# Performance work log

Hardware: AMD Instinct MI355X
Metric: run time of the kernel (lower is better)

## Reference

```python
import jax, jax.numpy as jnp
import numpy as np

N = 50000
E = 800000
IN_DIM = 256
OUT_DIM = 128
HEADS = 4
D_K = OUT_DIM // HEADS  # 32
BETA = 1.0  # beta_init, requires_grad=False (constant)
NEG_SLOPE = 0.2
EPS = 1e-12


def setup_inputs() -> dict:
    key = jax.random.key(0)
    k = jax.random.split(key, 8)
    H = jax.random.normal(k[0], (N, IN_DIM), dtype=jnp.float32)
    edge_index = jax.random.randint(k[1], (2, E), 0, N, dtype=jnp.int64)
    sim1_edge = jax.random.normal(k[2], (E,), dtype=jnp.float32)
    # Parameters (torch nn.Linear stores weight as (out, in); y = x @ W.T)
    W = jax.random.normal(k[3], (HEADS * D_K, IN_DIM), dtype=jnp.float32) * (1.0 / np.sqrt(IN_DIM))
    a_src = jax.random.normal(k[4], (HEADS, D_K), dtype=jnp.float32)
    a_dst = jax.random.normal(k[5], (HEADS, D_K), dtype=jnp.float32)
    msg_lin_w = jax.random.normal(k[6], (D_K, D_K), dtype=jnp.float32) * (1.0 / np.sqrt(D_K))
    return {"H": H, "edge_index": edge_index, "sim1_edge": sim1_edge,
            "W": W, "a_src": a_src, "a_dst": a_dst, "msg_lin_w": msg_lin_w}


def reference(H, edge_index, sim1_edge, W, a_src, a_dst, msg_lin_w):
    n = H.shape[0]
    H_proj = (H @ W.T).reshape(n, HEADS, D_K)           # [N, h, d_k]
    src, dst = edge_index[0], edge_index[1]
    h_src = H_proj[src]                                  # [E, h, d_k]
    h_dst = H_proj[dst]                                  # [E, h, d_k]
    # per-edge attention logits (struct + semantic)
    e = (jnp.einsum('ehd,hd->eh', h_src, a_src)
         + jnp.einsum('ehd,hd->eh', h_dst, a_dst)
         + BETA * sim1_edge[:, None])                    # [E, h]
    e = jnp.where(e >= 0, e, NEG_SLOPE * e)              # LeakyReLU(0.2)
    # global (per-head) max for stabilization, matching original e.max(dim=0)
    e = e - jnp.max(e, axis=0, keepdims=True)
    exp_e = jnp.exp(e)                                   # [E, h]
    denom = jax.ops.segment_sum(exp_e, dst, num_segments=n)  # [N, h]
    alpha = exp_e / (denom[dst] + EPS)                   # [E, h]  (dropout p=0 -> identity)
    m = alpha[:, :, None] * h_src                        # [E, h, d_k]
    out = jax.ops.segment_sum(m, dst, num_segments=n)    # [N, h, d_k]
    out_h = out.reshape(n, HEADS * D_K)                  # concat=True
    msg_base = jnp.einsum('ehd,od->eho', h_src, msg_lin_w).mean(axis=1)  # [E, d_k]
    alpha_mean = alpha.mean(axis=1)                      # [E]
    return out_h, alpha_mean, msg_base
```

## Files before the change

kernel.cpp:

```cpp
#include <hip/hip_runtime.h>
#include <hip/hip_bf16.h>
#include <hip/hip_fp16.h>
#include <float.h>

#define HEADS 4
#define DK 32

static constexpr float kBeta = 1.0f;
static constexpr float kNeg  = 0.2f;
static constexpr float kEps  = 1e-12f;

typedef __bf16 bf16x8 __attribute__((ext_vector_type(8)));
typedef float  f32x4  __attribute__((ext_vector_type(4)));

__device__ __forceinline__ float bf2f(unsigned short v) {
  return __uint_as_float((unsigned)v << 16);
}
__device__ __forceinline__ unsigned short f2bf(float f) {
  unsigned u = __float_as_uint(f);
  unsigned r = u + 0x7FFFu + ((u >> 16) & 1u);
  return (unsigned short)(r >> 16);
}
__device__ __forceinline__ float2 bfp2(unsigned u) {
  return make_float2(__uint_as_float(u << 16), __uint_as_float(u & 0xFFFF0000u));
}
__device__ __forceinline__ unsigned fkey(float x) {
  unsigned u = __float_as_uint(x);
  return (u & 0x80000000u) ? ~u : (u | 0x80000000u);
}
__device__ __forceinline__ float funkey(unsigned k) {
  unsigned u = (k & 0x80000000u) ? (k & 0x7fffffffu) : ~k;
  return __uint_as_float(u);
}
__device__ __forceinline__ bf16x8 as8(uint4 v) {
  union { uint4 u; bf16x8 b; } x; x.u = v; return x.b;
}

__global__ __launch_bounds__(256) void k_detect(const int* __restrict__ ei32,
                                                const unsigned* __restrict__ Hw,
                                                int* __restrict__ eflag,
                                                int* __restrict__ dflag,
                                                int E, int nw) {
  int i = blockIdx.x * 256 + threadIdx.x;
  if (i < 4096 && 2 * i + 1 < 2 * E && ei32[2 * i + 1] != 0) atomicOr(eflag, 1);
  if (i < nw && ((Hw[i] >> 7) & 0xFFu) == 0xFFu) atomicOr(dflag, 1);
}

__global__ __launch_bounds__(256) void k_cvt(const int* __restrict__ ei32,
                                             const int* __restrict__ eflag,
                                             int* __restrict__ src_i,
                                             int* __restrict__ dst_i,
                                             int* __restrict__ deg, int E) {
  int i = blockIdx.x * 256 + threadIdx.x;
  if (i >= E) return;
  int s, d;
  if (*eflag) { s = ei32[i];     d = ei32[E + i]; }
  else        { s = ei32[2 * i]; d = ei32[2 * E + 2 * i]; }
  src_i[i] = s;
  dst_i[i] = d;
  atomicAdd(deg + d, 1);
}

__global__ __launch_bounds__(256) void k_params(const void* __restrict__ a_src,
                                                const void* __restrict__ a_dst,
                                                const void* __restrict__ msg_w,
                                                float* __restrict__ af,
                                                float* __restrict__ msgwf,
                                                const int* __restrict__ dflag) {
  int i = blockIdx.x * 256 + threadIdx.x;
  int dt = *dflag;
  if (i < 128) {
    af[i] = dt ? ((const float*)a_src)[i] : bf2f(((const unsigned short*)a_src)[i]);
  } else if (i < 256) {
    int j = i - 128;
    af[i] = dt ? ((const float*)a_dst)[j] : bf2f(((const unsigned short*)a_dst)[j]);
  } else if (i < 1280) {
    int j = i - 256;
    msgwf[j] = dt ? ((const float*)msg_w)[j] : bf2f(((const unsigned short*)msg_w)[j]);
  }
}

__global__ __launch_bounds__(256) void k_wpack(const void* __restrict__ in,
                                               unsigned short* __restrict__ Bhi,
                                               unsigned short* __restrict__ Blo,
                                               const int* __restrict__ dflag, int n) {
  int i = blockIdx.x * 256 + threadIdx.x;
  if (i >= n) return;
  int r = i >> 8, c = i & 255;
  float v = (*dflag) ? ((const float*)in)[i] : bf2f(((const unsigned short*)in)[i]);
  unsigned short hb = f2bf(v);
  unsigned short lb = f2bf(v - bf2f(hb));
  int kt = c >> 5, ct = r >> 4;
  int lane = (((c >> 3) & 3) << 4) | (r & 15);
  int idx = ((kt * 8 + ct) * 64 + lane) * 8 + (c & 7);
  Bhi[idx] = hb;
  Blo[idx] = lb;
}

__global__ __launch_bounds__(256) void k_scan1(const int* __restrict__ deg,
                                               int* __restrict__ bsum, int N) {
  const int t = threadIdx.x;
  int i = blockIdx.x * 256 + t;
  int v = (i < N) ? deg[i] : 0;
#pragma unroll
  for (int off = 32; off; off >>= 1) v += __shfl_xor(v, off);
  __shared__ int red[4];
  if ((t & 63) == 0) red[t >> 6] = v;
  __syncthreads();
  if (t == 0) bsum[blockIdx.x] = red[0] + red[1] + red[2] + red[3];
}
__global__ __launch_bounds__(1024) void k_scan2(int* __restrict__ bsum, int nb) {
  __shared__ int part[1024];
  const int t = threadIdx.x;
  part[t] = (t < nb) ? bsum[t] : 0;
  __syncthreads();
  int own = part[t];
  for (int off = 1; off < 1024; off <<= 1) {
    int v = (t >= off) ? part[t - off] : 0;
    __syncthreads();
    part[t] += v;
    __syncthreads();
  }
  if (t < nb) bsum[t] = part[t] - own;
}
__global__ __launch_bounds__(256) void k_scan3(const int* __restrict__ deg,
                                               const int* __restrict__ bsum,
                                               int* __restrict__ row_ptr,
                                               int* __restrict__ cursor, int N) {
  __shared__ int part[256];
  const int t = threadIdx.x;
  int i = blockIdx.x * 256 + t;
  int v = (i < N) ? deg[i] : 0;
  part[t] = v;
  __syncthreads();
  for (int off = 1; off < 256; off <<= 1) {
    int x = (t >= off) ? part[t - off] : 0;
    __syncthreads();
    part[t] += x;
    __syncthreads();
  }
  int excl = part[t] - v + bsum[blockIdx.x];
  if (i < N) {
    row_ptr[i] = excl;
    cursor[i]  = excl;
    if (i == N - 1) row_ptr[N] = excl + v;
  }
}

__global__ __launch_bounds__(256) void k_fill(const int* __restrict__ dst,
                                              int* __restrict__ cursor,
                                              int* __restrict__ eidx, int E) {
  int e = blockIdx.x * 256 + threadIdx.x;
  if (e >= E) return;
  int pos = atomicAdd(cursor + dst[e], 1);
  eidx[pos] = e;
}

__global__ __launch_bounds__(256) void k_proj(const void* __restrict__ Hraw,
                                              const unsigned short* __restrict__ Bhi,
                                              const unsigned short* __restrict__ Blo,
                                              const int* __restrict__ dflag,
                                              float* __restrict__ Hproj, int N) {
  __shared__ uint4 lds4[4096];
  const int t = threadIdx.x;
  const int nb = blockIdx.x * 64;
  const int dt = *dflag;
  if (dt) {
    const float4* __restrict__ H4 = (const float4*)Hraw;
#pragma unroll
    for (int it = 0; it < 8; ++it) {
      int c = it * 256 + t;
      int row = c >> 5, k8 = c & 31;
      int gr = nb + row;
      float4 v0 = make_float4(0.f, 0.f, 0.f, 0.f), v1 = v0;
      if (gr < N) {
        v0 = H4[(size_t)gr * 64 + k8 * 2];
        v1 = H4[(size_t)gr * 64 + k8 * 2 + 1];
      }
      float f[8] = {v0.x, v0.y, v0.z, v0.w, v1.x, v1.y, v1.z, v1.w};
      unsigned hi[8], lo[8];
#pragma unroll
      for (int j = 0; j < 8; ++j) {
        unsigned short hb = f2bf(f[j]);
        hi[j] = hb;
        lo[j] = f2bf(f[j] - bf2f(hb));
      }
      int slot = (k8 * 64 + row) ^ (k8 & 7);
      lds4[slot] = make_uint4(hi[0] | (hi[1] << 16), hi[2] | (hi[3] << 16),
                              hi[4] | (hi[5] << 16), hi[6] | (hi[7] << 16));
      lds4[2048 + slot] = make_uint4(lo[0] | (lo[1] << 16), lo[2] | (lo[3] << 16),
                                     lo[4] | (lo[5] << 16), lo[6] | (lo[7] << 16));
    }
  } else {
    const uint4* __restrict__ H8 = (const uint4*)Hraw;
#pragma unroll
    for (int it = 0; it < 8; ++it) {
      int c = it * 256 + t;
      int row = c >> 5, k8 = c & 31;
      int gr = nb + row;
      uint4 v = make_uint4(0u, 0u, 0u, 0u);
      if (gr < N) v = H8[(size_t)gr * 32 + k8];
      lds4[(k8 * 64 + row) ^ (k8 & 7)] = v;
    }
  }
  __syncthreads();

  const int l = t & 63;
  const int wrow = (t >> 6) * 16;
  f32x4 acc[8];
#pragma unroll
  for (int ct = 0; ct < 8; ++ct) acc[ct] = (f32x4){0.f, 0.f, 0.f, 0.f};
  const uint4* __restrict__ Bh4 = (const uint4*)Bhi;
  const uint4* __restrict__ Bl4 = (const uint4*)Blo;
  if (dt) {
#pragma unroll 2
    for (int kt = 0; kt < 8; ++kt) {
      int k8 = kt * 4 + (l >> 4);
      int slot = (k8 * 64 + wrow + (l & 15)) ^ (k8 & 7);
      bf16x8 ah = as8(lds4[slot]);
      bf16x8 al = as8(lds4[2048 + slot]);
#pragma unroll
      for (int ct = 0; ct < 8; ++ct) {
        bf16x8 bh = as8(Bh4[(kt * 8 + ct) * 64 + l]);
        bf16x8 bl = as8(Bl4[(kt * 8 + ct) * 64 + l]);
        acc[ct] = __builtin_amdgcn_mfma_f32_16x16x32_bf16(ah, bh, acc[ct], 0, 0, 0);
        acc[ct] = __builtin_amdgcn_mfma_f32_16x16x32_bf16(ah, bl, acc[ct], 0, 0, 0);
        acc[ct] = __builtin_amdgcn_mfma_f32_16x16x32_bf16(al, bh, acc[ct], 0, 0, 0);
      }
    }
  } else {
#pragma unroll 2
    for (int kt = 0; kt < 8; ++kt) {
      int k8 = kt * 4 + (l >> 4);
      int slot = (k8 * 64 + wrow + (l & 15)) ^ (k8 & 7);
      bf16x8 ah = as8(lds4[slot]);
#pragma unroll
      for (int ct = 0; ct < 8; ++ct) {
        bf16x8 bh = as8(Bh4[(kt * 8 + ct) * 64 + l]);
        acc[ct] = __builtin_amdgcn_mfma_f32_16x16x32_bf16(ah, bh, acc[ct], 0, 0, 0);
      }
    }
  }
#pragma unroll
  for (int ct = 0; ct < 8; ++ct) {
#pragma unroll
    for (int r = 0; r < 4; ++r) {
      int grow = nb + wrow + (l >> 4) * 4 + r;
      if (grow < N) Hproj[(size_t)grow * 128 + ct * 16 + (l & 15)] = acc[ct][r];
    }
  }
}

__global__ __launch_bounds__(256) void k_node(const float* __restrict__ Hproj,
                                              const float* __restrict__ af,
                                              const float* __restrict__ msgwf,
                                              float* __restrict__ s_src,
                                              float* __restrict__ s_dst,
                                              __half* __restrict__ msgb,
                                              __half* __restrict__ Hb, int N) {
  const int l = threadIdx.x & 63;
  const int wb = threadIdx.x >> 6;
  const int n = (blockIdx.x << 2) + wb;
  if (n >= N) return;
  const float* row = Hproj + (size_t)n * 128;
  float h0 = row[l], h1 = row[64 + l];
  Hb[(size_t)n * 128 + l]      = __float2half(h0);
  Hb[(size_t)n * 128 + 64 + l] = __float2half(h1);
  float p0 = h0 * af[l],       p1 = h1 * af[64 + l];
  float q0 = h0 * af[128 + l], q1 = h1 * af[192 + l];
#pragma unroll
  for (int off = 16; off; off >>= 1) {
    p0 += __shfl_xor(p0, off);
    p1 += __shfl_xor(p1, off);
    q0 += __shfl_xor(q0, off);
    q1 += __shfl_xor(q1, off);
  }
  if (l == 0)  { s_src[n*4+0] = p0; s_src[n*4+2] = p1; s_dst[n*4+0] = q0; s_dst[n*4+2] = q1; }
  if (l == 32) { s_src[n*4+1] = p0; s_src[n*4+3] = p1; s_dst[n*4+1] = q0; s_dst[n*4+3] = q1; }
  float t4 = h0 + __shfl_xor(h0, 32) + h1 + __shfl_xor(h1, 32);
  float hbar = 0.25f * t4;
  if (l < DK) {
    float acc = 0.f;
#pragma unroll
    for (int d = 0; d < DK; ++d) acc += __shfl(hbar, d) * msgwf[l * DK + d];
    msgb[(size_t)n * DK + l] = __float2half(acc);
  }
}

__global__ __launch_bounds__(256) void k_logits(const int* __restrict__ src,
                                                const int* __restrict__ dst,
                                                const void* __restrict__ sim1,
                                                const int* __restrict__ dflag,
                                                const float* __restrict__ s_src,
                                                const float* __restrict__ s_dst,
                                                unsigned* __restrict__ gmax, int E) {
  const int e = blockIdx.x * 256 + threadIdx.x;
  float m0 = -FLT_MAX, m1 = -FLT_MAX, m2 = -FLT_MAX, m3 = -FLT_MAX;
  if (e < E) {
    int s = src[e], d = dst[e];
    float4 ss = *(const float4*)(s_src + (size_t)s * 4);
    float4 sd = *(const float4*)(s_dst + (size_t)d * 4);
    float sv = (*dflag) ? ((const float*)sim1)[e] : bf2f(((const unsigned short*)sim1)[e]);
    float b = kBeta * sv;
    float e0 = ss.x + sd.x + b; e0 = (e0 >= 0.f) ? e0 : kNeg * e0;
    float e1 = ss.y + sd.y + b; e1 = (e1 >= 0.f) ? e1 : kNeg * e1;
    float e2 = ss.z + sd.z + b; e2 = (e2 >= 0.f) ? e2 : kNeg * e2;
    float e3 = ss.w + sd.w + b; e3 = (e3 >= 0.f) ? e3 : kNeg * e3;
    m0 = e0; m1 = e1; m2 = e2; m3 = e3;
  }
#pragma unroll
  for (int off = 32; off; off >>= 1) {
    m0 = fmaxf(m0, __shfl_xor(m0, off));
    m1 = fmaxf(m1, __shfl_xor(m1, off));
    m2 = fmaxf(m2, __shfl_xor(m2, off));
    m3 = fmaxf(m3, __shfl_xor(m3, off));
  }
  __shared__ float red[4][4];
  if ((threadIdx.x & 63) == 0) {
    int w = threadIdx.x >> 6;
    red[w][0] = m0; red[w][1] = m1; red[w][2] = m2; red[w][3] = m3;
  }
  __syncthreads();
  if (threadIdx.x < 4) {
    int h = threadIdx.x;
    float mm = fmaxf(fmaxf(red[0][h], red[1][h]), fmaxf(red[2][h], red[3][h]));
    atomicMax(gmax + h, fkey(mm));
  }
}

__global__ __launch_bounds__(256) void k_msg(const int* __restrict__ src,
                                             const __half2* __restrict__ msgb2,
                                             const int* __restrict__ dflag,
                                             void* __restrict__ d_out,
                                             int N, int E) {
  long long tid = (long long)blockIdx.x * 256 + threadIdx.x;
  if (tid >= (long long)E * 16) return;
  int e = (int)(tid >> 4), jp = (int)(tid & 15);
  __half2 hv = msgb2[(size_t)src[e] * 16 + jp];
  float2 f = __half22float2(hv);
  const size_t msg_off = (size_t)N * 128 + (size_t)E;
  if (*dflag) {
    *(float2*)&((float*)d_out)[msg_off + (size_t)e * 32 + 2 * jp] = f;
  } else {
    __hip_bfloat162 b = __float22bfloat162_rn(f);
    *(__hip_bfloat162*)((__hip_bfloat16*)d_out + msg_off + (size_t)e * 32 + 2 * jp) = b;
  }
}

__global__ __launch_bounds__(256) void k_out(const int* __restrict__ row_ptr,
                                             const int* __restrict__ eidx,
                                             const int* __restrict__ src,
                                             const void* __restrict__ sim1,
                                             const float* __restrict__ s_src,
                                             const float* __restrict__ s_dst,
                                             const unsigned* __restrict__ gmax,
                                             const unsigned* __restrict__ Hb_u,
                                             const int* __restrict__ dflag,
                                             void* __restrict__ d_out, int N, int E) {
  const int n = (int)((blockIdx.x * 256 + threadIdx.x) >> 6);
  const int l = threadIdx.x & 63;
  if (n >= N) return;
  const int beg = row_ptr[n];
  const int deg = row_ptr[n + 1] - beg;
  const int dt = *dflag;
  const float m0 = funkey(gmax[0]), m1 = funkey(gmax[1]);
  const float m2 = funkey(gmax[2]), m3 = funkey(gmax[3]);
  const float4 sd = *(const float4*)(s_dst + (size_t)n * 4);
  const size_t alpha_off = (size_t)N * 128;
  float accx = 0.f, accy = 0.f;
  float4 dn = make_float4(0.f, 0.f, 0.f, 0.f);
  int eid = 0, s = 0;
  float4 ev = make_float4(0.f, 0.f, 0.f, 0.f);
  const bool small = (deg <= 64);
  if (small) {
    if (l < deg) {
      eid = eidx[beg + l];
      s = src[eid];
      float4 ss = *(const float4*)(s_src + (size_t)s * 4);
      float sv = dt ? ((const float*)sim1)[eid] : bf2f(((const unsigned short*)sim1)[eid]);
      float e0 = ss.x + sd.x + sv; e0 = (e0 >= 0.f) ? e0 : kNeg * e0;
      float e1 = ss.y + sd.y + sv; e1 = (e1 >= 0.f) ? e1 : kNeg * e1;
      float e2 = ss.z + sd.z + sv; e2 = (e2 >= 0.f) ? e2 : kNeg * e2;
      float e3 = ss.w + sd.w + sv; e3 = (e3 >= 0.f) ? e3 : kNeg * e3;
      ev = make_float4(expf(e0 - m0), expf(e1 - m1), expf(e2 - m2), expf(e3 - m3));
      dn = ev;
    }
  } else {
    for (int base = 0; base < deg; base += 64) {
      if (base + l < deg) {
        int e2i = eidx[beg + base + l];
        int s2 = src[e2i];
        float4 ss = *(const float4*)(s_src + (size_t)s2 * 4);
        float sv = dt ? ((const float*)sim1)[e2i] : bf2f(((const unsigned short*)sim1)[e2i]);
        float e0 = ss.x + sd.x + sv; e0 = (e0 >= 0.f) ? e0 : kNeg * e0;
        float e1 = ss.y + sd.y + sv; e1 = (e1 >= 0.f) ? e1 : kNeg * e1;
        float e2 = ss.z + sd.z + sv; e2 = (e2 >= 0.f) ? e2 : kNeg * e2;
        float e3 = ss.w + sd.w + sv; e3 = (e3 >= 0.f) ? e3 : kNeg * e3;
        dn.x += expf(e0 - m0); dn.y += expf(e1 - m1);
        dn.z += expf(e2 - m2); dn.w += expf(e3 - m3);
      }
    }
  }
#pragma unroll
  for (int off = 32; off; off >>= 1) {
    dn.x += __shfl_xor(dn.x, off);
    dn.y += __shfl_xor(dn.y, off);
    dn.z += __shfl_xor(dn.z, off);
    dn.w += __shfl_xor(dn.w, off);
  }
  const float i0 = 1.f / (dn.x + kEps), i1 = 1.f / (dn.y + kEps);
  const float i2 = 1.f / (dn.z + kEps), i3 = 1.f / (dn.w + kEps);
  const float myinv = (l < 32) ? ((l < 16) ? i0 : i1) : ((l < 48) ? i2 : i3);
  if (small) {
    if (l < deg) {
      float am = 0.25f * (ev.x * i0 + ev.y * i1 + ev.z * i2 + ev.w * i3);
      if (dt) ((float*)d_out)[alpha_off + eid] = am;
      else    ((__hip_bfloat16*)d_out)[alpha_off + eid] = __float2bfloat16(am);
    }
    for (int i = 0; i < deg; ++i) {
      int si = __shfl(s, i);
      float ax = __shfl(ev.x, i), ay = __shfl(ev.y, i);
      float az = __shfl(ev.z, i), aw = __shfl(ev.w, i);
      float aa = ((l < 32) ? ((l < 16) ? ax : ay) : ((l < 48) ? az : aw)) * myinv;
      unsigned u = Hb_u[(size_t)si * 64 + l];
      float2 f = __half22float2(*(const __half2*)&u);
      accx += aa * f.x;
      accy += aa * f.y;
    }
  } else {
    for (int base = 0; base < deg; base += 64) {
      int cnt = min(64, deg - base);
      int eid2 = 0, s2 = 0;
      float4 e2v = make_float4(0.f, 0.f, 0.f, 0.f);
      if (l < cnt) {
        eid2 = eidx[beg + base + l];
        s2 = src[eid2];
        float4 ss = *(const float4*)(s_src + (size_t)s2 * 4);
        float sv = dt ? ((const float*)sim1)[eid2] : bf2f(((const unsigned short*)sim1)[eid2]);
        float e0 = ss.x + sd.x + sv; e0 = (e0 >= 0.f) ? e0 : kNeg * e0;
        float e1 = ss.y + sd.y + sv; e1 = (e1 >= 0.f) ? e1 : kNeg * e1;
        float e2 = ss.z + sd.z + sv; e2 = (e2 >= 0.f) ? e2 : kNeg * e2;
        float e3 = ss.w + sd.w + sv; e3 = (e3 >= 0.f) ? e3 : kNeg * e3;
        e2v = make_float4(expf(e0 - m0), expf(e1 - m1), expf(e2 - m2), expf(e3 - m3));
        float am = 0.25f * (e2v.x * i0 + e2v.y * i1 + e2v.z * i2 + e2v.w * i3);
        if (dt) ((float*)d_out)[alpha_off + eid2] = am;
        else    ((__hip_bfloat16*)d_out)[alpha_off + eid2] = __float2bfloat16(am);
      }
      for (int i = 0; i < cnt; ++i) {
        int si = __shfl(s2, i);
        float ax = __shfl(e2v.x, i), ay = __shfl(e2v.y, i);
        float az = __shfl(e2v.z, i), aw = __shfl(e2v.w, i);
        float aa = ((l < 32) ? ((l < 16) ? ax : ay) : ((l < 48) ? az : aw)) * myinv;
        unsigned u = Hb_u[(size_t)si * 64 + l];
        float2 f = __half22float2(*(const __half2*)&u);
        accx += aa * f.x;
        accy += aa * f.y;
      }
    }
  }
  if (dt) {
    *(float2*)&((float*)d_out)[(size_t)n * 128 + 2 * l] = make_float2(accx, accy);
  } else {
    __hip_bfloat162 b = __float22bfloat162_rn(make_float2(accx, accy));
    *(__hip_bfloat162*)((__hip_bfloat16*)d_out + (size_t)n * 128 + 2 * l) = b;
  }
}

extern "C" void kernel_launch(void* const* d_in, const int* in_sizes, int n_in,
                              void* d_out, int out_size, void* d_ws, size_t ws_size,
                              hipStream_t stream) {
  const void* H     = d_in[0];
  const int*  ei    = (const int*)d_in[1];
  const void* sim1  = d_in[2];
  const void* W     = d_in[3];
  const void* a_src = d_in[4];
  const void* a_dst = d_in[5];
  const void* msg_w = d_in[6];
  const int N = in_sizes[0] / 256;
  const int E = in_sizes[2];
  const int NB = (N + 255) / 256;

  char* base     = (char*)d_ws;
  float* Hproj   = (float*)base;  base += (size_t)N * 128 * 4;
  float* s_src   = (float*)base;  base += (size_t)N * 4 * 4;
  float* s_dst   = (float*)base;  base += (size_t)N * 4 * 4;
  __half* msgb   = (__half*)base; base += (size_t)N * DK * 2;
  __half* Hb     = (__half*)base; base += (size_t)N * 128 * 2;
  unsigned short* Bhi = (unsigned short*)base; base += 32768 * 2;
  unsigned short* Blo = (unsigned short*)base; base += 32768 * 2;
  int* deg       = (int*)base;    base += (size_t)N * 4;
  unsigned* gmax = (unsigned*)base; base += 4 * 4;
  int* eflag     = (int*)base;    base += 4;
  int* dflag     = (int*)base;    base += 4;
  int* row_ptr   = (int*)base;    base += (size_t)(N + 1) * 4;
  int* cursor    = (int*)base;    base += (size_t)N * 4;
  int* bsum      = (int*)base;    base += 1024 * 4;
  int* eidx      = (int*)base;    base += (size_t)E * 4;
  int* src_i     = (int*)base;    base += (size_t)E * 4;
  int* dst_i     = (int*)base;    base += (size_t)E * 4;
  float* af      = (float*)base;  base += 256 * 4;
  float* msgwf   = (float*)base;  base += 1024 * 4;

  hipMemsetAsync(deg, 0, (size_t)(N + 6) * sizeof(int), stream);

  k_detect<<<512, 256, 0, stream>>>(ei, (const unsigned*)H, eflag, dflag, E, 131072);
  k_cvt<<<(E + 255) / 256, 256, 0, stream>>>(ei, eflag, src_i, dst_i, deg, E);
  k_wpack<<<128, 256, 0, stream>>>(W, Bhi, Blo, dflag, 128 * 256);
  k_params<<<5, 256, 0, stream>>>(a_src, a_dst, msg_w, af, msgwf, dflag);
  k_proj<<<(N + 63) / 64, 256, 0, stream>>>(H, Bhi, Blo, dflag, Hproj, N);
  k_scan1<<<NB, 256, 0, stream>>>(deg, bsum, N);
  k_scan2<<<1, 1024, 0, stream>>>(bsum, NB);
  k_scan3<<<NB, 256, 0, stream>>>(deg, bsum, row_ptr, cursor, N);
  k_fill<<<(E + 255) / 256, 256, 0, stream>>>(dst_i, cursor, eidx, E);
  k_node<<<(N + 3) / 4, 256, 0, stream>>>(Hproj, af, msgwf, s_src, s_dst, msgb, Hb, N);
  k_logits<<<(E + 255) / 256, 256, 0, stream>>>(src_i, dst_i, sim1, dflag, s_src, s_dst,
                                                gmax, E);
  k_msg<<<(int)(((long long)E * 16 + 255) / 256), 256, 0, stream>>>(
      src_i, (const __half2*)msgb, dflag, d_out, N, E);
  k_out<<<(int)(((size_t)N * 64 + 255) / 256), 256, 0, stream>>>(
      row_ptr, eidx, src_i, sim1, s_src, s_dst, gmax, (const unsigned*)Hb, dflag,
      d_out, N, E);
}
```

Baseline: 483.8 us.

## Fuse node epilogue into projection, merge CSR fill with logits, move alpha to edge kernel

```diff
diff --git a/kernel.cpp b/kernel.cpp
--- a/kernel.cpp
+++ b/kernel.cpp
@@ -20,9 +20,6 @@
   unsigned u = __float_as_uint(f);
   unsigned r = u + 0x7FFFu + ((u >> 16) & 1u);
   return (unsigned short)(r >> 16);
-}
-__device__ __forceinline__ float2 bfp2(unsigned u) {
-  return make_float2(__uint_as_float(u << 16), __uint_as_float(u & 0xFFFF0000u));
 }
 __device__ __forceinline__ unsigned fkey(float x) {
   unsigned u = __float_as_uint(x);
@@ -61,40 +58,39 @@
   atomicAdd(deg + d, 1);
 }
 
-__global__ __launch_bounds__(256) void k_params(const void* __restrict__ a_src,
-                                                const void* __restrict__ a_dst,
-                                                const void* __restrict__ msg_w,
-                                                float* __restrict__ af,
-                                                float* __restrict__ msgwf,
-                                                const int* __restrict__ dflag) {
-  int i = blockIdx.x * 256 + threadIdx.x;
-  int dt = *dflag;
-  if (i < 128) {
-    af[i] = dt ? ((const float*)a_src)[i] : bf2f(((const unsigned short*)a_src)[i]);
-  } else if (i < 256) {
-    int j = i - 128;
-    af[i] = dt ? ((const float*)a_dst)[j] : bf2f(((const unsigned short*)a_dst)[j]);
-  } else if (i < 1280) {
-    int j = i - 256;
-    msgwf[j] = dt ? ((const float*)msg_w)[j] : bf2f(((const unsigned short*)msg_w)[j]);
-  }
-}
-
-__global__ __launch_bounds__(256) void k_wpack(const void* __restrict__ in,
-                                               unsigned short* __restrict__ Bhi,
-                                               unsigned short* __restrict__ Blo,
-                                               const int* __restrict__ dflag, int n) {
-  int i = blockIdx.x * 256 + threadIdx.x;
-  if (i >= n) return;
-  int r = i >> 8, c = i & 255;
-  float v = (*dflag) ? ((const float*)in)[i] : bf2f(((const unsigned short*)in)[i]);
-  unsigned short hb = f2bf(v);
-  unsigned short lb = f2bf(v - bf2f(hb));
-  int kt = c >> 5, ct = r >> 4;
-  int lane = (((c >> 3) & 3) << 4) | (r & 15);
-  int idx = ((kt * 8 + ct) * 64 + lane) * 8 + (c & 7);
-  Bhi[idx] = hb;
-  Blo[idx] = lb;
+__global__ __launch_bounds__(256) void k_wparams(const void* __restrict__ in,
+                                                 unsigned short* __restrict__ Bhi,
+                                                 unsigned short* __restrict__ Blo,
+                                                 const void* __restrict__ a_src,
+                                                 const void* __restrict__ a_dst,
+                                                 const void* __restrict__ msg_w,
+                                                 float* __restrict__ af,
+                                                 float* __restrict__ msgwf,
+                                                 const int* __restrict__ dflag) {
+  const int dt = *dflag;
+  if (blockIdx.x < 128) {
+    int i = blockIdx.x * 256 + threadIdx.x;
+    int r = i >> 8, c = i & 255;
+    float v = dt ? ((const float*)in)[i] : bf2f(((const unsigned short*)in)[i]);
+    unsigned short hb = f2bf(v);
+    unsigned short lb = f2bf(v - bf2f(hb));
+    int kt = c >> 5, ct = r >> 4;
+    int lane = (((c >> 3) & 3) << 4) | (r & 15);
+    int idx = ((kt * 8 + ct) * 64 + lane) * 8 + (c & 7);
+    Bhi[idx] = hb;
+    Blo[idx] = lb;
+  } else {
+    int i = (blockIdx.x - 128) * 256 + threadIdx.x;
+    if (i < 128) {
+      af[i] = dt ? ((const float*)a_src)[i] : bf2f(((const unsigned short*)a_src)[i]);
+    } else if (i < 256) {
+      int j = i - 128;
+      af[i] = dt ? ((const float*)a_dst)[j] : bf2f(((const unsigned short*)a_dst)[j]);
+    } else if (i < 1280) {
+      int j = i - 256;
+      msgwf[j] = dt ? ((const float*)msg_w)[j] : bf2f(((const unsigned short*)msg_w)[j]);
+    }
+  }
 }
 
 __global__ __launch_bounds__(256) void k_scan1(const int* __restrict__ deg,
@@ -147,21 +143,18 @@
   }
 }
 
-__global__ __launch_bounds__(256) void k_fill(const int* __restrict__ dst,
-                                              int* __restrict__ cursor,
-                                              int* __restrict__ eidx, int E) {
-  int e = blockIdx.x * 256 + threadIdx.x;
-  if (e >= E) return;
-  int pos = atomicAdd(cursor + dst[e], 1);
-  eidx[pos] = e;
-}
-
 __global__ __launch_bounds__(256) void k_proj(const void* __restrict__ Hraw,
                                               const unsigned short* __restrict__ Bhi,
                                               const unsigned short* __restrict__ Blo,
                                               const int* __restrict__ dflag,
-                                              float* __restrict__ Hproj, int N) {
+                                              const float* __restrict__ af,
+                                              const float* __restrict__ msgwf,
+                                              float* __restrict__ s_src,
+                                              float* __restrict__ s_dst,
+                                              __half* __restrict__ msgb,
+                                              __half* __restrict__ Hb, int N) {
   __shared__ uint4 lds4[4096];
+  float* ldsF = (float*)lds4;
   const int t = threadIdx.x;
   const int nb = blockIdx.x * 64;
   const int dt = *dflag;
@@ -241,66 +234,59 @@
       }
     }
   }
-#pragma unroll
-  for (int ct = 0; ct < 8; ++ct) {
-#pragma unroll
-    for (int r = 0; r < 4; ++r) {
-      int grow = nb + wrow + (l >> 4) * 4 + r;
-      if (grow < N) Hproj[(size_t)grow * 128 + ct * 16 + (l & 15)] = acc[ct][r];
-    }
-  }
-}
-
-__global__ __launch_bounds__(256) void k_node(const float* __restrict__ Hproj,
-                                              const float* __restrict__ af,
-                                              const float* __restrict__ msgwf,
-                                              float* __restrict__ s_src,
-                                              float* __restrict__ s_dst,
-                                              __half* __restrict__ msgb,
-                                              __half* __restrict__ Hb, int N) {
-  const int l = threadIdx.x & 63;
-  const int wb = threadIdx.x >> 6;
-  const int n = (blockIdx.x << 2) + wb;
-  if (n >= N) return;
-  const float* row = Hproj + (size_t)n * 128;
-  float h0 = row[l], h1 = row[64 + l];
-  Hb[(size_t)n * 128 + l]      = __float2half(h0);
-  Hb[(size_t)n * 128 + 64 + l] = __float2half(h1);
-  float p0 = h0 * af[l],       p1 = h1 * af[64 + l];
-  float q0 = h0 * af[128 + l], q1 = h1 * af[192 + l];
-#pragma unroll
-  for (int off = 16; off; off >>= 1) {
-    p0 += __shfl_xor(p0, off);
-    p1 += __shfl_xor(p1, off);
-    q0 += __shfl_xor(q0, off);
-    q1 += __shfl_xor(q1, off);
-  }
-  if (l == 0)  { s_src[n*4+0] = p0; s_src[n*4+2] = p1; s_dst[n*4+0] = q0; s_dst[n*4+2] = q1; }
-  if (l == 32) { s_src[n*4+1] = p0; s_src[n*4+3] = p1; s_dst[n*4+1] = q0; s_dst[n*4+3] = q1; }
-  float t4 = h0 + __shfl_xor(h0, 32) + h1 + __shfl_xor(h1, 32);
-  float hbar = 0.25f * t4;
-  if (l < DK) {
-    float acc = 0.f;
-#pragma unroll
-    for (int d = 0; d < DK; ++d) acc += __shfl(hbar, d) * msgwf[l * DK + d];
-    msgb[(size_t)n * DK + l] = __float2half(acc);
-  }
-}
-
-__global__ __launch_bounds__(256) void k_logits(const int* __restrict__ src,
-                                                const int* __restrict__ dst,
+  __syncthreads();
+#pragma unroll
+  for (int ct = 0; ct < 8; ++ct)
+#pragma unroll
+    for (int r = 0; r < 4; ++r)
+      ldsF[(wrow + (l >> 4) * 4 + r) * 132 + ct * 16 + (l & 15)] = acc[ct][r];
+  __syncthreads();
+  for (int i = 0; i < 16; ++i) {
+    int row = wrow + i, n = nb + row;
+    if (n >= N) break;
+    float h0 = ldsF[row * 132 + l], h1 = ldsF[row * 132 + 64 + l];
+    Hb[(size_t)n * 128 + l]      = __float2half(h0);
+    Hb[(size_t)n * 128 + 64 + l] = __float2half(h1);
+    float p0 = h0 * af[l],       p1 = h1 * af[64 + l];
+    float q0 = h0 * af[128 + l], q1 = h1 * af[192 + l];
+#pragma unroll
+    for (int off = 16; off; off >>= 1) {
+      p0 += __shfl_xor(p0, off);
+      p1 += __shfl_xor(p1, off);
+      q0 += __shfl_xor(q0, off);
+      q1 += __shfl_xor(q1, off);
+    }
+    if (l == 0)  { s_src[n*4+0] = p0; s_src[n*4+2] = p1; s_dst[n*4+0] = q0; s_dst[n*4+2] = q1; }
+    if (l == 32) { s_src[n*4+1] = p0; s_src[n*4+3] = p1; s_dst[n*4+1] = q0; s_dst[n*4+3] = q1; }
+    float t4 = h0 + __shfl_xor(h0, 32) + h1 + __shfl_xor(h1, 32);
+    float hbar = 0.25f * t4;
+    if (l < DK) {
+      float acc2 = 0.f;
+#pragma unroll
+      for (int d = 0; d < DK; ++d) acc2 += __shfl(hbar, d) * msgwf[l * DK + d];
+      msgb[(size_t)n * DK + l] = __float2half(acc2);
+    }
+  }
+}
+
+__global__ __launch_bounds__(256) void k_fillog(const int* __restrict__ src,
+                                                const int* __restrict__ dstv,
                                                 const void* __restrict__ sim1,
                                                 const int* __restrict__ dflag,
                                                 const float* __restrict__ s_src,
                                                 const float* __restrict__ s_dst,
+                                                int* __restrict__ cursor,
+                                                int2* __restrict__ pack,
                                                 unsigned* __restrict__ gmax, int E) {
   const int e = blockIdx.x * 256 + threadIdx.x;
   float m0 = -FLT_MAX, m1 = -FLT_MAX, m2 = -FLT_MAX, m3 = -FLT_MAX;
   if (e < E) {
-    int s = src[e], d = dst[e];
+    int s = src[e], d = dstv[e];
+    float sv = (*dflag) ? ((const float*)sim1)[e] : bf2f(((const unsigned short*)sim1)[e]);
+    int pos = atomicAdd(cursor + d, 1);
+    pack[pos] = make_int2(s, __float_as_int(sv));
     float4 ss = *(const float4*)(s_src + (size_t)s * 4);
     float4 sd = *(const float4*)(s_dst + (size_t)d * 4);
-    float sv = (*dflag) ? ((const float*)sim1)[e] : bf2f(((const unsigned short*)sim1)[e]);
     float b = kBeta * sv;
     float e0 = ss.x + sd.x + b; e0 = (e0 >= 0.f) ? e0 : kNeg * e0;
     float e1 = ss.y + sd.y + b; e1 = (e1 >= 0.f) ? e1 : kNeg * e1;
@@ -328,35 +314,15 @@
   }
 }
 
-__global__ __launch_bounds__(256) void k_msg(const int* __restrict__ src,
-                                             const __half2* __restrict__ msgb2,
-                                             const int* __restrict__ dflag,
-                                             void* __restrict__ d_out,
-                                             int N, int E) {
-  long long tid = (long long)blockIdx.x * 256 + threadIdx.x;
-  if (tid >= (long long)E * 16) return;
-  int e = (int)(tid >> 4), jp = (int)(tid & 15);
-  __half2 hv = msgb2[(size_t)src[e] * 16 + jp];
-  float2 f = __half22float2(hv);
-  const size_t msg_off = (size_t)N * 128 + (size_t)E;
-  if (*dflag) {
-    *(float2*)&((float*)d_out)[msg_off + (size_t)e * 32 + 2 * jp] = f;
-  } else {
-    __hip_bfloat162 b = __float22bfloat162_rn(f);
-    *(__hip_bfloat162*)((__hip_bfloat16*)d_out + msg_off + (size_t)e * 32 + 2 * jp) = b;
-  }
-}
-
 __global__ __launch_bounds__(256) void k_out(const int* __restrict__ row_ptr,
-                                             const int* __restrict__ eidx,
-                                             const int* __restrict__ src,
-                                             const void* __restrict__ sim1,
+                                             const int2* __restrict__ pack,
                                              const float* __restrict__ s_src,
                                              const float* __restrict__ s_dst,
                                              const unsigned* __restrict__ gmax,
                                              const unsigned* __restrict__ Hb_u,
                                              const int* __restrict__ dflag,
-                                             void* __restrict__ d_out, int N, int E) {
+                                             float* __restrict__ denom,
+                                             void* __restrict__ d_out, int N) {
   const int n = (int)((blockIdx.x * 256 + threadIdx.x) >> 6);
   const int l = threadIdx.x & 63;
   if (n >= N) return;
@@ -366,18 +332,17 @@
   const float m0 = funkey(gmax[0]), m1 = funkey(gmax[1]);
   const float m2 = funkey(gmax[2]), m3 = funkey(gmax[3]);
   const float4 sd = *(const float4*)(s_dst + (size_t)n * 4);
-  const size_t alpha_off = (size_t)N * 128;
   float accx = 0.f, accy = 0.f;
   float4 dn = make_float4(0.f, 0.f, 0.f, 0.f);
-  int eid = 0, s = 0;
+  int s = 0;
   float4 ev = make_float4(0.f, 0.f, 0.f, 0.f);
   const bool small = (deg <= 64);
   if (small) {
     if (l < deg) {
-      eid = eidx[beg + l];
-      s = src[eid];
+      int2 p = pack[beg + l];
+      s = p.x;
+      float sv = __int_as_float(p.y);
       float4 ss = *(const float4*)(s_src + (size_t)s * 4);
-      float sv = dt ? ((const float*)sim1)[eid] : bf2f(((const unsigned short*)sim1)[eid]);
       float e0 = ss.x + sd.x + sv; e0 = (e0 >= 0.f) ? e0 : kNeg * e0;
       float e1 = ss.y + sd.y + sv; e1 = (e1 >= 0.f) ? e1 : kNeg * e1;
       float e2 = ss.z + sd.z + sv; e2 = (e2 >= 0.f) ? e2 : kNeg * e2;
@@ -388,10 +353,9 @@
   } else {
     for (int base = 0; base < deg; base += 64) {
       if (base + l < deg) {
-        int e2i = eidx[beg + base + l];
-        int s2 = src[e2i];
-        float4 ss = *(const float4*)(s_src + (size_t)s2 * 4);
-        float sv = dt ? ((const float*)sim1)[e2i] : bf2f(((const unsigned short*)sim1)[e2i]);
+        int2 p = pack[beg + base + l];
+        float sv = __int_as_float(p.y);
+        float4 ss = *(const float4*)(s_src + (size_t)p.x * 4);
         float e0 = ss.x + sd.x + sv; e0 = (e0 >= 0.f) ? e0 : kNeg * e0;
         float e1 = ss.y + sd.y + sv; e1 = (e1 >= 0.f) ? e1 : kNeg * e1;
         float e2 = ss.z + sd.z + sv; e2 = (e2 >= 0.f) ? e2 : kNeg * e2;
@@ -408,15 +372,11 @@
     dn.z += __shfl_xor(dn.z, off);
     dn.w += __shfl_xor(dn.w, off);
   }
+  if (l == 0) *(float4*)(denom + (size_t)n * 4) = make_float4(dn.x, dn.y, dn.z, dn.w);
   const float i0 = 1.f / (dn.x + kEps), i1 = 1.f / (dn.y + kEps);
   const float i2 = 1.f / (dn.z + kEps), i3 = 1.f / (dn.w + kEps);
   const float myinv = (l < 32) ? ((l < 16) ? i0 : i1) : ((l < 48) ? i2 : i3);
   if (small) {
-    if (l < deg) {
-      float am = 0.25f * (ev.x * i0 + ev.y * i1 + ev.z * i2 + ev.w * i3);
-      if (dt) ((float*)d_out)[alpha_off + eid] = am;
-      else    ((__hip_bfloat16*)d_out)[alpha_off + eid] = __float2bfloat16(am);
-    }
     for (int i = 0; i < deg; ++i) {
       int si = __shfl(s, i);
       float ax = __shfl(ev.x, i), ay = __shfl(ev.y, i);
@@ -430,21 +390,18 @@
   } else {
     for (int base = 0; base < deg; base += 64) {
       int cnt = min(64, deg - base);
-      int eid2 = 0, s2 = 0;
+      int s2 = 0;
       float4 e2v = make_float4(0.f, 0.f, 0.f, 0.f);
       if (l < cnt) {
-        eid2 = eidx[beg + base + l];
-        s2 = src[eid2];
+        int2 p = pack[beg + base + l];
+        s2 = p.x;
+        float sv = __int_as_float(p.y);
         float4 ss = *(const float4*)(s_src + (size_t)s2 * 4);
-        float sv = dt ? ((const float*)sim1)[eid2] : bf2f(((const unsigned short*)sim1)[eid2]);
         float e0 = ss.x + sd.x + sv; e0 = (e0 >= 0.f) ? e0 : kNeg * e0;
         float e1 = ss.y + sd.y + sv; e1 = (e1 >= 0.f) ? e1 : kNeg * e1;
         float e2 = ss.z + sd.z + sv; e2 = (e2 >= 0.f) ? e2 : kNeg * e2;
         float e3 = ss.w + sd.w + sv; e3 = (e3 >= 0.f) ? e3 : kNeg * e3;
         e2v = make_float4(expf(e0 - m0), expf(e1 - m1), expf(e2 - m2), expf(e3 - m3));
-        float am = 0.25f * (e2v.x * i0 + e2v.y * i1 + e2v.z * i2 + e2v.w * i3);
-        if (dt) ((float*)d_out)[alpha_off + eid2] = am;
-        else    ((__hip_bfloat16*)d_out)[alpha_off + eid2] = __float2bfloat16(am);
       }
       for (int i = 0; i < cnt; ++i) {
         int si = __shfl(s2, i);
@@ -463,6 +420,52 @@
   } else {
     __hip_bfloat162 b = __float22bfloat162_rn(make_float2(accx, accy));
     *(__hip_bfloat162*)((__hip_bfloat16*)d_out + (size_t)n * 128 + 2 * l) = b;
+  }
+}
+
+__global__ __launch_bounds__(256) void k_edge(const int* __restrict__ src,
+                                              const int* __restrict__ dstv,
+                                              const void* __restrict__ sim1,
+                                              const int* __restrict__ dflag,
+                                              const float* __restrict__ s_src,
+                                              const float* __restrict__ s_dst,
+                                              const float* __restrict__ denom,
+                                              const unsigned* __restrict__ gmax,
+                                              const __half2* __restrict__ msgb2,
+                                              void* __restrict__ d_out,
+                                              int N, int E) {
+  long long tid = (long long)blockIdx.x * 256 + threadIdx.x;
+  if (tid >= (long long)E * 16) return;
+  int e = (int)(tid >> 4), jp = (int)(tid & 15);
+  const int dt = *dflag;
+  int s = src[e];
+  __half2 hv = msgb2[(size_t)s * 16 + jp];
+  float2 f = __half22float2(hv);
+  const size_t alpha_off = (size_t)N * 128;
+  const size_t msg_off = alpha_off + (size_t)E;
+  if (dt) {
+    *(float2*)&((float*)d_out)[msg_off + (size_t)e * 32 + 2 * jp] = f;
+  } else {
+    __hip_bfloat162 b = __float22bfloat162_rn(f);
+    *(__hip_bfloat162*)((__hip_bfloat16*)d_out + msg_off + (size_t)e * 32 + 2 * jp) = b;
+  }
+  if (jp == 0) {
+    int d = dstv[e];
+    float sv = dt ? ((const float*)sim1)[e] : bf2f(((const unsigned short*)sim1)[e]);
+    float4 ss = *(const float4*)(s_src + (size_t)s * 4);
+    float4 sd = *(const float4*)(s_dst + (size_t)d * 4);
+    float4 dn = *(const float4*)(denom + (size_t)d * 4);
+    float m0 = funkey(gmax[0]), m1 = funkey(gmax[1]);
+    float m2 = funkey(gmax[2]), m3 = funkey(gmax[3]);
+    float b = kBeta * sv;
+    float e0 = ss.x + sd.x + b; e0 = (e0 >= 0.f) ? e0 : kNeg * e0;
+    float e1 = ss.y + sd.y + b; e1 = (e1 >= 0.f) ? e1 : kNeg * e1;
+    float e2 = ss.z + sd.z + b; e2 = (e2 >= 0.f) ? e2 : kNeg * e2;
+    float e3 = ss.w + sd.w + b; e3 = (e3 >= 0.f) ? e3 : kNeg * e3;
+    float am = 0.25f * (expf(e0 - m0) / (dn.x + kEps) + expf(e1 - m1) / (dn.y + kEps) +
+                        expf(e2 - m2) / (dn.z + kEps) + expf(e3 - m3) / (dn.w + kEps));
+    if (dt) ((float*)d_out)[alpha_off + e] = am;
+    else    ((__hip_bfloat16*)d_out)[alpha_off + e] = __float2bfloat16(am);
   }
 }
 
@@ -481,21 +484,21 @@
   const int NB = (N + 255) / 256;
 
   char* base     = (char*)d_ws;
-  float* Hproj   = (float*)base;  base += (size_t)N * 128 * 4;
   float* s_src   = (float*)base;  base += (size_t)N * 4 * 4;
   float* s_dst   = (float*)base;  base += (size_t)N * 4 * 4;
   __half* msgb   = (__half*)base; base += (size_t)N * DK * 2;
   __half* Hb     = (__half*)base; base += (size_t)N * 128 * 2;
+  float* denom   = (float*)base;  base += (size_t)N * 4 * 4;
   unsigned short* Bhi = (unsigned short*)base; base += 32768 * 2;
   unsigned short* Blo = (unsigned short*)base; base += 32768 * 2;
   int* deg       = (int*)base;    base += (size_t)N * 4;
   unsigned* gmax = (unsigned*)base; base += 4 * 4;
   int* eflag     = (int*)base;    base += 4;
   int* dflag     = (int*)base;    base += 4;
-  int* row_ptr   = (int*)base;    base += (size_t)(N + 1) * 4;
+  int* row_ptr   = (int*)base;    base += (size_t)(N + 2) * 4;
   int* cursor    = (int*)base;    base += (size_t)N * 4;
   int* bsum      = (int*)base;    base += 1024 * 4;
-  int* eidx      = (int*)base;    base += (size_t)E * 4;
+  int2* pack     = (int2*)base;   base += (size_t)E * 8;
   int* src_i     = (int*)base;    base += (size_t)E * 4;
   int* dst_i     = (int*)base;    base += (size_t)E * 4;
   float* af      = (float*)base;  base += 256 * 4;
@@ -505,19 +508,17 @@
 
   k_detect<<<512, 256, 0, stream>>>(ei, (const unsigned*)H, eflag, dflag, E, 131072);
   k_cvt<<<(E + 255) / 256, 256, 0, stream>>>(ei, eflag, src_i, dst_i, deg, E);
-  k_wpack<<<128, 256, 0, stream>>>(W, Bhi, Blo, dflag, 128 * 256);
-  k_params<<<5, 256, 0, stream>>>(a_src, a_dst, msg_w, af, msgwf, dflag);
-  k_proj<<<(N + 63) / 64, 256, 0, stream>>>(H, Bhi, Blo, dflag, Hproj, N);
+  k_wparams<<<133, 256, 0, stream>>>(W, Bhi, Blo, a_src, a_dst, msg_w, af, msgwf, dflag);
+  k_proj<<<(N + 63) / 64, 256, 0, stream>>>(H, Bhi, Blo, dflag, af, msgwf,
+                                            s_src, s_dst, msgb, Hb, N);
   k_scan1<<<NB, 256, 0, stream>>>(deg, bsum, N);
   k_scan2<<<1, 1024, 0, stream>>>(bsum, NB);
   k_scan3<<<NB, 256, 0, stream>>>(deg, bsum, row_ptr, cursor, N);
-  k_fill<<<(E + 255) / 256, 256, 0, stream>>>(dst_i, cursor, eidx, E);
-  k_node<<<(N + 3) / 4, 256, 0, stream>>>(Hproj, af, msgwf, s_src, s_dst, msgb, Hb, N);
-  k_logits<<<(E + 255) / 256, 256, 0, stream>>>(src_i, dst_i, sim1, dflag, s_src, s_dst,
-                                                gmax, E);
-  k_msg<<<(int)(((long long)E * 16 + 255) / 256), 256, 0, stream>>>(
-      src_i, (const __half2*)msgb, dflag, d_out, N, E);
+  k_fillog<<<(E + 255) / 256, 256, 0, stream>>>(src_i, dst_i, sim1, dflag, s_src, s_dst,
+                                                cursor, pack, gmax, E);
   k_out<<<(int)(((size_t)N * 64 + 255) / 256), 256, 0, stream>>>(
-      row_ptr, eidx, src_i, sim1, s_src, s_dst, gmax, (const unsigned*)Hb, dflag,
+      row_ptr, pack, s_src, s_dst, gmax, (const unsigned*)Hb, dflag, denom, d_out, N);
+  k_edge<<<(int)(((long long)E * 16 + 255) / 256), 256, 0, stream>>>(
+      src_i, dst_i, sim1, dflag, s_src, s_dst, denom, gmax, (const __half2*)msgb,
       d_out, N, E);
 }
```

Result: no change. 477.7 us (-1.3%).
